# Kernel optimization log

Hardware: AMD Instinct MI355X
Metric: run time of the kernel (lower is better)

## Reference

```python
import jax, jax.numpy as jnp
import numpy as np

N_NODES = 8192
N_EDGES = 524288
D_IN = 256
D_OUT = 256


def setup_inputs() -> dict:
    key = jax.random.key(0)
    ks = jax.random.split(key, 8)
    h = jax.random.normal(ks[0], (N_NODES, D_IN), dtype=jnp.float32)
    # Xavier-uniform-like scale for weights
    s = (6.0 / (D_IN + D_OUT)) ** 0.5
    W = jax.random.uniform(ks[1], (D_IN, D_OUT), jnp.float32, -s, s)
    Wq = jax.random.uniform(ks[2], (D_IN, D_OUT), jnp.float32, -s, s)
    bq = jnp.zeros((D_OUT,), jnp.float32)
    Wk = jax.random.uniform(ks[3], (D_IN, D_OUT), jnp.float32, -s, s)
    bk = jnp.zeros((D_OUT,), jnp.float32)
    senders = jax.random.randint(ks[4], (N_EDGES,), 0, N_NODES, dtype=jnp.int64 if jax.config.jax_enable_x64 else jnp.int32)
    receivers = jax.random.randint(ks[5], (N_EDGES,), 0, N_NODES, dtype=jnp.int64 if jax.config.jax_enable_x64 else jnp.int32)
    return {"h": h, "W": W, "Wq": Wq, "bq": bq, "Wk": Wk, "bk": bk,
            "senders": senders, "receivers": receivers}


def reference(h, W, Wq, bq, Wk, bk, senders, receivers):
    # Projected node features: (N, D_OUT)
    h_proj = jnp.dot(h, W)
    # Dense attention logits a = q @ k^T: (N, N), as in the original module
    q = jnp.dot(h, Wq) + bq
    k = jnp.dot(h, Wk) + bk
    a = jnp.dot(q, k.T)
    # Gather per-edge messages and attention weights, weight, scatter-add
    messages = h_proj[senders] * a[senders, receivers][:, None]  # (E, D_OUT)
    aggregated = jax.ops.segment_sum(messages, receivers, num_segments=h.shape[0])
    return jax.nn.relu(aggregated)
```

## Files before the change

kernel.cpp:

```cpp
#include <hip/hip_runtime.h>
#include <stdint.h>

typedef unsigned short u16;
typedef unsigned int u32;
typedef short v8s __attribute__((ext_vector_type(8)));
typedef float v4f __attribute__((ext_vector_type(4)));

#define N_NODES 8192
#define N_EDGES 524288
#define DFEAT 256
#define PADC 160

static __device__ __forceinline__ float bflo(u32 u) { return __uint_as_float(u << 16); }
static __device__ __forceinline__ float bfhi(u32 u) { return __uint_as_float(u & 0xffff0000u); }
static __device__ __forceinline__ u16 f2bf(float f) {
    u32 u = __float_as_uint(f);
    return (u16)((u + 0x7fffu + ((u >> 16) & 1u)) >> 16);
}

__global__ void prep_small(const float* __restrict__ w0, const float* __restrict__ w1,
                           const float* __restrict__ w2, u16* __restrict__ wt,
                           int* __restrict__ cnt) {
    int b = blockIdx.x;
    if (b < 48) {
        __shared__ u16 t[64][65];
        int region = b >> 4, tile = b & 15;
        int k0 = (tile >> 2) * 64, n0 = (tile & 3) * 64;
        const float* w = (region == 0) ? w0 : ((region == 1) ? w1 : w2);
        int tx = threadIdx.x & 63, ty = threadIdx.x >> 6;
#pragma unroll
        for (int it = 0; it < 16; it++) {
            int row = it * 4 + ty;
            t[row][tx] = f2bf(w[(k0 + row) * 256 + n0 + tx]);
        }
        __syncthreads();
        u16* o = wt + region * 65536;
#pragma unroll
        for (int it = 0; it < 16; it++) {
            int row = it * 4 + ty;
            o[(n0 + row) * 256 + k0 + tx] = t[tx][row];
        }
    } else {
        int i = ((b - 48) * 256 + threadIdx.x) * 4;
        *(int4*)(cnt + i) = make_int4(0, 0, 0, 0);
    }
}

__global__ __launch_bounds__(256) void scatter_k(
    const int* __restrict__ recv, const int* __restrict__ send,
    int* __restrict__ cnt, u16* __restrict__ es) {
    int e = (blockIdx.x * 256 + threadIdx.x) * 4;
    int4 rv = *(const int4*)(recv + e);
    int4 sv = *(const int4*)(send + e);
    int r, s, pos;
    r = rv.x; s = sv.x; pos = atomicAdd(&cnt[r], 1); if (pos < PADC) es[r * PADC + pos] = (u16)s;
    r = rv.y; s = sv.y; pos = atomicAdd(&cnt[r], 1); if (pos < PADC) es[r * PADC + pos] = (u16)s;
    r = rv.z; s = sv.z; pos = atomicAdd(&cnt[r], 1); if (pos < PADC) es[r * PADC + pos] = (u16)s;
    r = rv.w; s = sv.w; pos = atomicAdd(&cnt[r], 1); if (pos < PADC) es[r * PADC + pos] = (u16)s;
}

__global__ __launch_bounds__(256) void gemm_k(
    const float* __restrict__ h, const u16* __restrict__ wt,
    const float* __restrict__ bq, const float* __restrict__ bk,
    u16* __restrict__ hproj, u16* __restrict__ qbuf, u16* __restrict__ kbuf) {
    int g = blockIdx.x;
    int wave = threadIdx.x >> 6, lane = threadIdx.x & 63;
    int lm = lane & 15, lq = lane >> 4;
    int bx = g & 127, by = g >> 7;
    int m0 = bx * 64 + wave * 16;
    int region = by >> 2, n0b = (by & 3) * 64;
    const u16* wtr = wt + region * 65536;

    v4f acc[4];
#pragma unroll
    for (int nt = 0; nt < 4; nt++) acc[nt] = (v4f){0.f, 0.f, 0.f, 0.f};

    const float* arow = h + (m0 + lm) * 256 + lq * 8;
#pragma unroll
    for (int k0 = 0; k0 < 256; k0 += 32) {
        float4 f0 = *(const float4*)(arow + k0);
        float4 f1 = *(const float4*)(arow + k0 + 4);
        v8s a;
        a[0] = (short)f2bf(f0.x); a[1] = (short)f2bf(f0.y);
        a[2] = (short)f2bf(f0.z); a[3] = (short)f2bf(f0.w);
        a[4] = (short)f2bf(f1.x); a[5] = (short)f2bf(f1.y);
        a[6] = (short)f2bf(f1.z); a[7] = (short)f2bf(f1.w);
#pragma unroll
        for (int nt = 0; nt < 4; nt++) {
            v8s bb = *(const v8s*)(wtr + (n0b + nt * 16 + lm) * 256 + k0 + lq * 8);
            acc[nt] = __builtin_amdgcn_mfma_f32_16x16x32_bf16(a, bb, acc[nt], 0, 0, 0);
        }
    }
    u16* outp = (region == 0) ? hproj : ((region == 1) ? qbuf : kbuf);
    const float* bias = (region == 1) ? bq : ((region == 2) ? bk : nullptr);
#pragma unroll
    for (int nt = 0; nt < 4; nt++) {
        int nn = n0b + nt * 16 + lm;
        float bv = bias ? bias[nn] : 0.f;
#pragma unroll
        for (int i = 0; i < 4; i++) {
            int m = m0 + lq * 4 + i;
            outp[m * 256 + nn] = f2bf(acc[nt][i] + bv);
        }
    }
}

#define DOT_AGG(SIDX) do {                                                    \
    int off_ = (int)(SIDX) * 256 + cb;                                        \
    uint4 qv_ = *(const uint4*)(qbuf + off_);                                 \
    uint4 hv_ = *(const uint4*)(hpb + off_);                                  \
    float p_ = kr0 * bflo(qv_.x) + kr1 * bfhi(qv_.x)                          \
             + kr2 * bflo(qv_.y) + kr3 * bfhi(qv_.y)                          \
             + kr4 * bflo(qv_.z) + kr5 * bfhi(qv_.z)                          \
             + kr6 * bflo(qv_.w) + kr7 * bfhi(qv_.w);                         \
    p_ += __shfl_xor(p_, 1, 32);                                              \
    p_ += __shfl_xor(p_, 2, 32);                                              \
    p_ += __shfl_xor(p_, 4, 32);                                              \
    p_ += __shfl_xor(p_, 8, 32);                                              \
    p_ += __shfl_xor(p_, 16, 32);                                             \
    a0 += p_ * bflo(hv_.x); a1 += p_ * bfhi(hv_.x);                           \
    a2 += p_ * bflo(hv_.y); a3 += p_ * bfhi(hv_.y);                           \
    a4 += p_ * bflo(hv_.z); a5 += p_ * bfhi(hv_.z);                           \
    a6 += p_ * bflo(hv_.w); a7 += p_ * bfhi(hv_.w);                           \
} while (0)

__global__ __launch_bounds__(256, 4) void edge_fused(
    const u16* __restrict__ qbuf, const u16* __restrict__ kbuf,
    const u16* __restrict__ hpb, const int* __restrict__ cnt,
    const u16* __restrict__ es, float* __restrict__ out) {
    int wave = threadIdx.x >> 6, lane = threadIdx.x & 63;
    int r = blockIdx.x * 4 + wave;
    int lh = lane & 31, half = lane >> 5;
    int cb = lh * 8;
    int n = min(cnt[r], PADC);
    int base = r * PADC;

    uint4 kv = *(const uint4*)(kbuf + r * 256 + cb);
    float kr0 = bflo(kv.x), kr1 = bfhi(kv.x), kr2 = bflo(kv.y), kr3 = bfhi(kv.y),
          kr4 = bflo(kv.z), kr5 = bfhi(kv.z), kr6 = bflo(kv.w), kr7 = bfhi(kv.w);

    float a0 = 0.f, a1 = 0.f, a2 = 0.f, a3 = 0.f,
          a4 = 0.f, a5 = 0.f, a6 = 0.f, a7 = 0.f;

    uint2 sp = *(const uint2*)(es + base + half * 4);
    for (int c0 = 0; c0 < n; c0 += 8) {
        int nx = c0 + 8;
        uint2 spn = sp;
        if (nx < n) spn = *(const uint2*)(es + base + nx + half * 4);

        if (nx <= n) {
            DOT_AGG(sp.x & 0xffffu);
            DOT_AGG(sp.x >> 16);
            DOT_AGG(sp.y & 0xffffu);
            DOT_AGG(sp.y >> 16);
        } else {
            int mrem = n - c0 - half * 4;
            if (mrem > 0) DOT_AGG(sp.x & 0xffffu);
            if (mrem > 1) DOT_AGG(sp.x >> 16);
            if (mrem > 2) DOT_AGG(sp.y & 0xffffu);
            if (mrem > 3) DOT_AGG(sp.y >> 16);
        }
        sp = spn;
    }

    a0 += __shfl_xor(a0, 32, 64); a1 += __shfl_xor(a1, 32, 64);
    a2 += __shfl_xor(a2, 32, 64); a3 += __shfl_xor(a3, 32, 64);
    a4 += __shfl_xor(a4, 32, 64); a5 += __shfl_xor(a5, 32, 64);
    a6 += __shfl_xor(a6, 32, 64); a7 += __shfl_xor(a7, 32, 64);

    if (half == 0) {
        float4 o0, o1;
        o0.x = fmaxf(a0, 0.f); o0.y = fmaxf(a1, 0.f);
        o0.z = fmaxf(a2, 0.f); o0.w = fmaxf(a3, 0.f);
        o1.x = fmaxf(a4, 0.f); o1.y = fmaxf(a5, 0.f);
        o1.z = fmaxf(a6, 0.f); o1.w = fmaxf(a7, 0.f);
        float* op = out + r * 256 + cb;
        *(float4*)op = o0;
        *(float4*)(op + 4) = o1;
    }
}

extern "C" void kernel_launch(void* const* d_in, const int* in_sizes, int n_in,
                              void* d_out, int out_size, void* d_ws, size_t ws_size,
                              hipStream_t stream) {
    const float* h  = (const float*)d_in[0];
    const float* W  = (const float*)d_in[1];
    const float* Wq = (const float*)d_in[2];
    const float* bq = (const float*)d_in[3];
    const float* Wk = (const float*)d_in[4];
    const float* bk = (const float*)d_in[5];
    const int* senders   = (const int*)d_in[6];
    const int* receivers = (const int*)d_in[7];
    float* out = (float*)d_out;

    char* ws = (char*)d_ws;
    u16* wt    = (u16*)ws;
    u16* hproj = (u16*)(ws + 393216);
    u16* qbuf  = hproj + N_NODES * DFEAT;
    u16* kbuf  = qbuf + N_NODES * DFEAT;
    int* cnt   = (int*)(kbuf + N_NODES * DFEAT);
    u16* es    = (u16*)(cnt + N_NODES);

    prep_small<<<56, 256, 0, stream>>>(W, Wq, Wk, wt, cnt);
    scatter_k<<<512, 256, 0, stream>>>(receivers, senders, cnt, es);
    gemm_k<<<1536, 256, 0, stream>>>(h, wt, bq, bk, hproj, qbuf, kbuf);
    edge_fused<<<N_NODES / 4, 256, 0, stream>>>(qbuf, kbuf, hproj, cnt, es, out);
}
```

Measured before the change: 187.1 us.

## Merge edge scatter with projection GEMM and batch gathers in edge loop

Folds the edge-bucketing scatter and the three-way projection GEMM into one launch: the first 2048 blocks scatter one edge per thread and the remaining blocks run the MFMA GEMM, so the two independent stages can overlap and one launch is saved. In the edge aggregation loop, the four q/hproj gathers per iteration are issued together before the dot products, and the four butterfly shuffle reductions are interleaved, to expose more memory- and ALU-level parallelism. This raises register pressure in the edge kernel, which is limited by launch bounds to four blocks per SM, and mixes heterogeneous block types in one grid.

```diff
diff --git a/kernel.cpp b/kernel.cpp
--- a/kernel.cpp
+++ b/kernel.cpp
@@ -46,82 +46,85 @@
     }
 }
 
-__global__ __launch_bounds__(256) void scatter_k(
-    const int* __restrict__ recv, const int* __restrict__ send,
-    int* __restrict__ cnt, u16* __restrict__ es) {
-    int e = (blockIdx.x * 256 + threadIdx.x) * 4;
-    int4 rv = *(const int4*)(recv + e);
-    int4 sv = *(const int4*)(send + e);
-    int r, s, pos;
-    r = rv.x; s = sv.x; pos = atomicAdd(&cnt[r], 1); if (pos < PADC) es[r * PADC + pos] = (u16)s;
-    r = rv.y; s = sv.y; pos = atomicAdd(&cnt[r], 1); if (pos < PADC) es[r * PADC + pos] = (u16)s;
-    r = rv.z; s = sv.z; pos = atomicAdd(&cnt[r], 1); if (pos < PADC) es[r * PADC + pos] = (u16)s;
-    r = rv.w; s = sv.w; pos = atomicAdd(&cnt[r], 1); if (pos < PADC) es[r * PADC + pos] = (u16)s;
-}
-
-__global__ __launch_bounds__(256) void gemm_k(
+__global__ __launch_bounds__(256) void main_mid(
     const float* __restrict__ h, const u16* __restrict__ wt,
     const float* __restrict__ bq, const float* __restrict__ bk,
-    u16* __restrict__ hproj, u16* __restrict__ qbuf, u16* __restrict__ kbuf) {
-    int g = blockIdx.x;
-    int wave = threadIdx.x >> 6, lane = threadIdx.x & 63;
-    int lm = lane & 15, lq = lane >> 4;
-    int bx = g & 127, by = g >> 7;
-    int m0 = bx * 64 + wave * 16;
-    int region = by >> 2, n0b = (by & 3) * 64;
-    const u16* wtr = wt + region * 65536;
-
-    v4f acc[4];
-#pragma unroll
-    for (int nt = 0; nt < 4; nt++) acc[nt] = (v4f){0.f, 0.f, 0.f, 0.f};
-
-    const float* arow = h + (m0 + lm) * 256 + lq * 8;
-#pragma unroll
-    for (int k0 = 0; k0 < 256; k0 += 32) {
-        float4 f0 = *(const float4*)(arow + k0);
-        float4 f1 = *(const float4*)(arow + k0 + 4);
-        v8s a;
-        a[0] = (short)f2bf(f0.x); a[1] = (short)f2bf(f0.y);
-        a[2] = (short)f2bf(f0.z); a[3] = (short)f2bf(f0.w);
-        a[4] = (short)f2bf(f1.x); a[5] = (short)f2bf(f1.y);
-        a[6] = (short)f2bf(f1.z); a[7] = (short)f2bf(f1.w);
+    const int* __restrict__ recv, const int* __restrict__ send,
+    u16* __restrict__ hproj, u16* __restrict__ qbuf, u16* __restrict__ kbuf,
+    int* __restrict__ cnt, u16* __restrict__ es) {
+    int b = blockIdx.x;
+    if (b < 2048) {
+        int e = b * 256 + threadIdx.x;
+        int r = recv[e];
+        int s = send[e];
+        int pos = atomicAdd(&cnt[r], 1);
+        if (pos < PADC) es[r * PADC + pos] = (u16)s;
+    } else {
+        int g = b - 2048;
+        int wave = threadIdx.x >> 6, lane = threadIdx.x & 63;
+        int lm = lane & 15, lq = lane >> 4;
+        int bx = g & 127, by = g >> 7;
+        int m0 = bx * 64 + wave * 16;
+        int region = by >> 2, n0b = (by & 3) * 64;
+        const u16* wtr = wt + region * 65536;
+
+        v4f acc[4];
+#pragma unroll
+        for (int nt = 0; nt < 4; nt++) acc[nt] = (v4f){0.f, 0.f, 0.f, 0.f};
+
+        const float* arow = h + (m0 + lm) * 256 + lq * 8;
+#pragma unroll
+        for (int k0 = 0; k0 < 256; k0 += 32) {
+            float4 f0 = *(const float4*)(arow + k0);
+            float4 f1 = *(const float4*)(arow + k0 + 4);
+            v8s a;
+            a[0] = (short)f2bf(f0.x); a[1] = (short)f2bf(f0.y);
+            a[2] = (short)f2bf(f0.z); a[3] = (short)f2bf(f0.w);
+            a[4] = (short)f2bf(f1.x); a[5] = (short)f2bf(f1.y);
+            a[6] = (short)f2bf(f1.z); a[7] = (short)f2bf(f1.w);
+#pragma unroll
+            for (int nt = 0; nt < 4; nt++) {
+                v8s bb = *(const v8s*)(wtr + (n0b + nt * 16 + lm) * 256 + k0 + lq * 8);
+                acc[nt] = __builtin_amdgcn_mfma_f32_16x16x32_bf16(a, bb, acc[nt], 0, 0, 0);
+            }
+        }
+        u16* outp = (region == 0) ? hproj : ((region == 1) ? qbuf : kbuf);
+        const float* bias = (region == 1) ? bq : ((region == 2) ? bk : nullptr);
 #pragma unroll
         for (int nt = 0; nt < 4; nt++) {
-            v8s bb = *(const v8s*)(wtr + (n0b + nt * 16 + lm) * 256 + k0 + lq * 8);
-            acc[nt] = __builtin_amdgcn_mfma_f32_16x16x32_bf16(a, bb, acc[nt], 0, 0, 0);
-        }
-    }
-    u16* outp = (region == 0) ? hproj : ((region == 1) ? qbuf : kbuf);
-    const float* bias = (region == 1) ? bq : ((region == 2) ? bk : nullptr);
-#pragma unroll
-    for (int nt = 0; nt < 4; nt++) {
-        int nn = n0b + nt * 16 + lm;
-        float bv = bias ? bias[nn] : 0.f;
-#pragma unroll
-        for (int i = 0; i < 4; i++) {
-            int m = m0 + lq * 4 + i;
-            outp[m * 256 + nn] = f2bf(acc[nt][i] + bv);
-        }
-    }
-}
-
-#define DOT_AGG(SIDX) do {                                                    \
+            int nn = n0b + nt * 16 + lm;
+            float bv = bias ? bias[nn] : 0.f;
+#pragma unroll
+            for (int i = 0; i < 4; i++) {
+                int m = m0 + lq * 4 + i;
+                outp[m * 256 + nn] = f2bf(acc[nt][i] + bv);
+            }
+        }
+    }
+}
+
+
+#define DOT8(Q) (kr0 * bflo((Q).x) + kr1 * bfhi((Q).x)                        \
+               + kr2 * bflo((Q).y) + kr3 * bfhi((Q).y)                        \
+               + kr4 * bflo((Q).z) + kr5 * bfhi((Q).z)                        \
+               + kr6 * bflo((Q).w) + kr7 * bfhi((Q).w))
+
+#define AXPY(P, H) do {                                                       \
+    a0 += (P) * bflo((H).x); a1 += (P) * bfhi((H).x);                         \
+    a2 += (P) * bflo((H).y); a3 += (P) * bfhi((H).y);                         \
+    a4 += (P) * bflo((H).z); a5 += (P) * bfhi((H).z);                         \
+    a6 += (P) * bflo((H).w); a7 += (P) * bfhi((H).w);                         \
+} while (0)
+
+#define DOT_AGG1(SIDX) do {                                                   \
     int off_ = (int)(SIDX) * 256 + cb;                                        \
     uint4 qv_ = *(const uint4*)(qbuf + off_);                                 \
     uint4 hv_ = *(const uint4*)(hpb + off_);                                  \
-    float p_ = kr0 * bflo(qv_.x) + kr1 * bfhi(qv_.x)                          \
-             + kr2 * bflo(qv_.y) + kr3 * bfhi(qv_.y)                          \
-             + kr4 * bflo(qv_.z) + kr5 * bfhi(qv_.z)                          \
-             + kr6 * bflo(qv_.w) + kr7 * bfhi(qv_.w);                         \
-    p_ += __shfl_xor(p_, 1, 32);                                              \
-    p_ += __shfl_xor(p_, 2, 32);                                              \
-    p_ += __shfl_xor(p_, 4, 32);                                              \
-    p_ += __shfl_xor(p_, 8, 32);                                              \
+    float p_ = DOT8(qv_);                                                     \
+    p_ += __shfl_xor(p_, 1, 32);  p_ += __shfl_xor(p_, 2, 32);                \
+    p_ += __shfl_xor(p_, 4, 32);  p_ += __shfl_xor(p_, 8, 32);                \
     p_ += __shfl_xor(p_, 16, 32);                                             \
-    a0 += p_ * bflo(hv_.x); a1 += p_ * bfhi(hv_.x);                           \
-    a2 += p_ * bflo(hv_.y); a3 += p_ * bfhi(hv_.y);                           \
-    a4 += p_ * bflo(hv_.z); a5 += p_ * bfhi(hv_.z);                           \
-    a6 += p_ * bflo(hv_.w); a7 += p_ * bfhi(hv_.w);                           \
+    AXPY(p_, hv_);                                                            \
 } while (0)
 
 __global__ __launch_bounds__(256, 4) void edge_fused(
@@ -149,16 +152,42 @@
         if (nx < n) spn = *(const uint2*)(es + base + nx + half * 4);
 
         if (nx <= n) {
-            DOT_AGG(sp.x & 0xffffu);
-            DOT_AGG(sp.x >> 16);
-            DOT_AGG(sp.y & 0xffffu);
-            DOT_AGG(sp.y >> 16);
+            int s0 = (int)(sp.x & 0xffffu), s1 = (int)(sp.x >> 16);
+            int s2 = (int)(sp.y & 0xffffu), s3 = (int)(sp.y >> 16);
+            int o0 = s0 * 256 + cb, o1 = s1 * 256 + cb;
+            int o2 = s2 * 256 + cb, o3 = s3 * 256 + cb;
+            uint4 q0 = *(const uint4*)(qbuf + o0);
+            uint4 q1 = *(const uint4*)(qbuf + o1);
+            uint4 q2 = *(const uint4*)(qbuf + o2);
+            uint4 q3 = *(const uint4*)(qbuf + o3);
+            uint4 h0 = *(const uint4*)(hpb + o0);
+            uint4 h1 = *(const uint4*)(hpb + o1);
+            uint4 h2 = *(const uint4*)(hpb + o2);
+            uint4 h3 = *(const uint4*)(hpb + o3);
+            float p0 = DOT8(q0);
+            float p1 = DOT8(q1);
+            float p2 = DOT8(q2);
+            float p3 = DOT8(q3);
+            p0 += __shfl_xor(p0, 1, 32);  p1 += __shfl_xor(p1, 1, 32);
+            p2 += __shfl_xor(p2, 1, 32);  p3 += __shfl_xor(p3, 1, 32);
+            p0 += __shfl_xor(p0, 2, 32);  p1 += __shfl_xor(p1, 2, 32);
+            p2 += __shfl_xor(p2, 2, 32);  p3 += __shfl_xor(p3, 2, 32);
+            p0 += __shfl_xor(p0, 4, 32);  p1 += __shfl_xor(p1, 4, 32);
+            p2 += __shfl_xor(p2, 4, 32);  p3 += __shfl_xor(p3, 4, 32);
+            p0 += __shfl_xor(p0, 8, 32);  p1 += __shfl_xor(p1, 8, 32);
+            p2 += __shfl_xor(p2, 8, 32);  p3 += __shfl_xor(p3, 8, 32);
+            p0 += __shfl_xor(p0, 16, 32); p1 += __shfl_xor(p1, 16, 32);
+            p2 += __shfl_xor(p2, 16, 32); p3 += __shfl_xor(p3, 16, 32);
+            AXPY(p0, h0);
+            AXPY(p1, h1);
+            AXPY(p2, h2);
+            AXPY(p3, h3);
         } else {
             int mrem = n - c0 - half * 4;
-            if (mrem > 0) DOT_AGG(sp.x & 0xffffu);
-            if (mrem > 1) DOT_AGG(sp.x >> 16);
-            if (mrem > 2) DOT_AGG(sp.y & 0xffffu);
-            if (mrem > 3) DOT_AGG(sp.y >> 16);
+            if (mrem > 0) DOT_AGG1(sp.x & 0xffffu);
+            if (mrem > 1) DOT_AGG1(sp.x >> 16);
+            if (mrem > 2) DOT_AGG1(sp.y & 0xffffu);
+            if (mrem > 3) DOT_AGG1(sp.y >> 16);
         }
         sp = spn;
     }
@@ -202,7 +231,7 @@
     u16* es    = (u16*)(cnt + N_NODES);
 
     prep_small<<<56, 256, 0, stream>>>(W, Wq, Wk, wt, cnt);
-    scatter_k<<<512, 256, 0, stream>>>(receivers, senders, cnt, es);
-    gemm_k<<<1536, 256, 0, stream>>>(h, wt, bq, bk, hproj, qbuf, kbuf);
+    main_mid<<<3584, 256, 0, stream>>>(h, wt, bq, bk, receivers, senders,
+                                       hproj, qbuf, kbuf, cnt, es);
     edge_fused<<<N_NODES / 4, 256, 0, stream>>>(qbuf, kbuf, hproj, cnt, es, out);
 }
```

Measured after the change: 182.2 us. 1.03x faster.
